# Kernel optimization log

Hardware: AMD Instinct MI355X
Metric: run time of the kernel (lower is better)

The kernel has to match this reference:

```python
import jax, jax.numpy as jnp
import numpy as np

# H2RConfig constants
KERNEL = 3
MAX_ROUTES = 1000
STRIDE = 4.0
MIN_SIZE = 32.0
MAX_SIZE = 512.0
SCORE_POWER = 2.0
UNC_WEIGHT = 0.35


def setup_inputs() -> dict:
    key = jax.random.key(0)
    k1, k2, k3 = jax.random.split(key, 3)
    shape = (32, 1, 512, 512)  # [B, 1, H, W] heatmaps at stride 4
    return {
        "route_logits": jax.random.normal(k1, shape, jnp.float32),
        "scale_logits": jax.random.normal(k2, shape, jnp.float32),
        "uncertainty_logits": jax.random.normal(k3, shape, jnp.float32),
        "image_h": 2048,
        "image_w": 2048,
    }


def reference(route_logits, scale_logits, uncertainty_logits, image_h, image_w):
    # score map: sigmoid^power, modulated by uncertainty (use_route_uncertainty=True)
    score = jnp.power(jax.nn.sigmoid(route_logits), SCORE_POWER)
    score = score * (1.0 - UNC_WEIGHT * jax.nn.sigmoid(uncertainty_logits))

    # local-max NMS: 3x3 max pool, stride 1, SAME padding (torch pads with -inf)
    pooled = jax.lax.reduce_window(
        score, -jnp.inf, jax.lax.max,
        window_dimensions=(1, 1, KERNEL, KERNEL),
        window_strides=(1, 1, 1, 1),
        padding="SAME",
    )
    peak_mask = score == pooled
    filtered = jnp.where(peak_mask, score, -1.0)

    B = score.shape[0]
    Wd = score.shape[3]
    flat = filtered.reshape(B, -1)                 # [B, H*W]
    values, indices = jax.lax.top_k(flat, MAX_ROUTES)  # [B, K]
    valid = values > 0.0                            # torch drops these; we mask/pad

    ys = indices // Wd
    xs = indices % Wd
    cx = (xs.astype(jnp.float32) + 0.5) * STRIDE
    cy = (ys.astype(jnp.float32) + 0.5) * STRIDE

    # gather scale / uncertainty at peak locations
    sc = jnp.take_along_axis(scale_logits.reshape(B, -1), indices, axis=1)
    un = jax.nn.sigmoid(jnp.take_along_axis(uncertainty_logits.reshape(B, -1), indices, axis=1))

    side = MIN_SIZE + jax.nn.sigmoid(sc) * (MAX_SIZE - MIN_SIZE)
    side = side * (1.0 + 0.25 * un)
    half = side * 0.5

    iw = float(image_w)
    ih = float(image_h)
    x1 = jnp.clip(cx - half, 0.0, iw - 1.0)
    y1 = jnp.clip(cy - half, 0.0, ih - 1.0)
    x2 = jnp.clip(cx + half, 1.0, iw)
    y2 = jnp.clip(cy + half, 1.0, ih)

    bcol = jnp.broadcast_to(jnp.arange(B, dtype=jnp.float32)[:, None], values.shape)
    rois = jnp.stack([bcol, x1, y1, x2, y2], axis=-1)  # [B, K, 5]

    # padded (fixed-shape) equivalent of torch's variable-length concat
    rois = jnp.where(valid[..., None], rois, 0.0)
    scores = jnp.where(valid, values, 0.0)
    return rois, scores, valid
```

## Files before the change

### kernel.cpp

```cpp
#include <hip/hip_runtime.h>
#include <hip/hip_bf16.h>
#include <math.h>


#define B_   32
#define H_   512
#define W_   512
#define HW_  (H_ * W_)
#define K_   1000
#define ROWS_ 16
#define THR_  512
#define NSTRIP_ 32
#define WSEGCAP_ 176
#define STRIPCAP_ (8 * WSEGCAP_)
#define NSLOT_ (NSTRIP_ * STRIPCAP_)
#define NPAIR_ (NSLOT_ / 2)
#define NBUK_ 4096
#define NW2_  (NBUK_ / 2)
#define GCAP_ 2048
#define HOTCAP_ 896
#define HOTPAIR_ (NSTRIP_ * HOTCAP_ / 2)
#define HOTBITS_ 0x3F000000u

#define PL_BYTES_  ((size_t)B_ * NSLOT_ * 8)
#define GH2_BYTES_ ((size_t)B_ * NSTRIP_ * NW2_ * 4)
#define HL_BYTES_  ((size_t)B_ * NSTRIP_ * HOTCAP_ * 8)

__device__ __forceinline__ float np_expf(float x) {
#pragma clang fp contract(off)
    const float log2e = 1.44269504088896341f;
    float z = x * log2e;
    float m = rintf(z);
    float r = fmaf(m, -0.693359375f, x);
    r = fmaf(m, 2.12194440e-4f, r);
    float r2 = r * r;
    float p = fmaf(1.9875691500e-4f, r, 1.3981999507e-3f);
    p = fmaf(p, r, 8.3334519073e-3f);
    p = fmaf(p, r, 4.1665795894e-2f);
    p = fmaf(p, r, 1.6666665459e-1f);
    p = fmaf(p, r, 5.0000001201e-1f);
    p = fmaf(p, r2, r);
    p = p + 1.0f;
    int mi = (int)m;
    float sc = __int_as_float((127 + mi) << 23);
    return p * sc;
}

__device__ __forceinline__ float sigmoid_np(float x) {
#pragma clang fp contract(off)
    float e = np_expf(-x);
    float d = 1.0f + e;
    return 1.0f / d;
}

__device__ __forceinline__ float score_ref(float r, float u) {
#pragma clang fp contract(off)
    float s  = sigmoid_np(r);
    float s2 = s * s;
    float su = sigmoid_np(u);
    float t  = 0.35f * su;
    float m  = 1.0f - t;
    return s2 * m;
}

__device__ __forceinline__ float sigmoid_fast(float x) {
    return 1.0f / (1.0f + __expf(-x));
}

__global__ __launch_bounds__(THR_, 4) void fused_peak_kernel(
    const float* __restrict__ route, const float* __restrict__ unc,
    unsigned long long* __restrict__ plist,
    unsigned int* __restrict__ ghist2,
    unsigned long long* __restrict__ hotlist)
{
    __shared__ float sm[ROWS_ + 2][W_];
    __shared__ int hcnt;

    const int tid   = threadIdx.x;
    const int lane  = tid & 63;
    const int wid   = tid >> 6;
    const int strip = blockIdx.x;
    const int b     = blockIdx.y;
    const int r0    = strip * ROWS_;
    if (tid == 0) hcnt = 0;

    const float4* rb4 = (const float4*)(route + (size_t)b * HW_);
    const float4* ub4 = (const float4*)(unc   + (size_t)b * HW_);
    unsigned long long* wseg =
        plist + (size_t)(b * NSTRIP_ + strip) * STRIPCAP_ + wid * WSEGCAP_;
    unsigned long long* hseg =
        hotlist + (size_t)(b * NSTRIP_ + strip) * HOTCAP_;

    float4 rv[5], uv[5];
    int lrow[5], c4[5]; bool ok[5];
    #pragma unroll
    for (int k = 0; k < 5; ++k) {
        int slot = tid + k * THR_;
        slot = slot < 2303 ? slot : 2303;
        int row = slot >> 7;
        int gy  = r0 - 1 + row;
        lrow[k] = row; c4[k] = slot & 127;
        ok[k]   = (gy >= 0 && gy < H_);
        int cy  = gy < 0 ? 0 : (gy >= H_ ? H_ - 1 : gy);
        rv[k] = rb4[cy * 128 + c4[k]];
        uv[k] = ub4[cy * 128 + c4[k]];
    }
    #pragma unroll
    for (int k = 0; k < 5; ++k) {
        float4 s;
        s.x = score_ref(rv[k].x, uv[k].x);
        s.y = score_ref(rv[k].y, uv[k].y);
        s.z = score_ref(rv[k].z, uv[k].z);
        s.w = score_ref(rv[k].w, uv[k].w);
        if (!ok[k]) { s.x = -INFINITY; s.y = -INFINITY;
                      s.z = -INFINITY; s.w = -INFINITY; }
        *(float4*)&sm[lrow[k]][c4[k] * 4] = s;
    }
    __syncthreads();

    const unsigned long long lt = (1ull << lane) - 1ull;
    int wn = 0;
    unsigned int hreg[8];
    #pragma unroll
    for (int j = 0; j < 4; ++j) {
        int g  = tid + j * THR_;
        int ly = 1 + (g >> 7);
        int x0 = (g & 127) * 4;
        int gy = r0 + (ly - 1);
        float4 q0 = *(const float4*)&sm[ly - 1][x0];
        float4 q1 = *(const float4*)&sm[ly    ][x0];
        float4 q2 = *(const float4*)&sm[ly + 1][x0];
        bool hasL = (x0 > 0), hasR = (x0 + 4 < W_);
        float l0 = hasL ? sm[ly - 1][x0 - 1] : -INFINITY;
        float l1 = hasL ? sm[ly    ][x0 - 1] : -INFINITY;
        float l2 = hasL ? sm[ly + 1][x0 - 1] : -INFINITY;
        float e0 = hasR ? sm[ly - 1][x0 + 4] : -INFINITY;
        float e1 = hasR ? sm[ly    ][x0 + 4] : -INFINITY;
        float e2 = hasR ? sm[ly + 1][x0 + 4] : -INFINITY;
        float f_m1 = fmaxf(l0, fmaxf(l1, l2));
        float f_0  = fmaxf(q0.x, fmaxf(q1.x, q2.x));
        float f_1  = fmaxf(q0.y, fmaxf(q1.y, q2.y));
        float f_2  = fmaxf(q0.z, fmaxf(q1.z, q2.z));
        float f_3  = fmaxf(q0.w, fmaxf(q1.w, q2.w));
        float f_4  = fmaxf(e0, fmaxf(e1, e2));
        float tb0  = fmaxf(q0.x, q2.x);
        float tb1  = fmaxf(q0.y, q2.y);
        float tb2  = fmaxf(q0.z, q2.z);
        float tb3  = fmaxf(q0.w, q2.w);
        float vv[4] = { q1.x, q1.y, q1.z, q1.w };
        float mm[4];
        mm[0] = fmaxf(fmaxf(f_m1, f_1), tb0);
        mm[1] = fmaxf(fmaxf(f_0,  f_2), tb1);
        mm[2] = fmaxf(fmaxf(f_1,  f_3), tb2);
        mm[3] = fmaxf(fmaxf(f_2,  f_4), tb3);
        unsigned int pk01 = 0u, pk23 = 0u;
        #pragma unroll
        for (int i = 0; i < 4; ++i) {
            bool take = (vv[i] >= mm[i]);
            unsigned long long mk = __ballot(take);
            int p = wn + __popcll(mk & lt);
            bool stored = take && (p < WSEGCAP_);
            unsigned int bits = __float_as_uint(vv[i]);
            unsigned long long key = 0ull;
            if (stored) {
                unsigned int idx = (unsigned int)(gy * W_ + x0 + i);
                key = ((unsigned long long)bits << 32)
                      | (0xFFFFFFFFu - idx);
                wseg[p] = key;
                unsigned int bkt = bits >> 18;
                if (i < 2) pk01 |= bkt << (16 * i);
                else       pk23 |= bkt << (16 * (i - 2));
            }
            bool hot = stored && (bits >= HOTBITS_);
            unsigned long long hmk = __ballot(hot);
            if (hmk) {
                int ldr = __ffsll(hmk) - 1;
                int hb = 0;
                if (lane == ldr) hb = atomicAdd(&hcnt, __popcll(hmk));
                hb = __shfl(hb, ldr, 64);
                if (hot) {
                    int hp = hb + __popcll(hmk & lt);
                    if (hp < HOTCAP_) hseg[hp] = key;
                }
            }
            wn += __popcll(mk);
        }
        hreg[2 * j]     = pk01;
        hreg[2 * j + 1] = pk23;
    }
    for (int i = (wn < WSEGCAP_ ? wn : WSEGCAP_) + lane; i < WSEGCAP_; i += 64)
        wseg[i] = 0ull;
    __syncthreads();

    {
        int hn = hcnt < HOTCAP_ ? hcnt : HOTCAP_;
        for (int i = hn + tid; i < HOTCAP_; i += THR_) hseg[i] = 0ull;
    }

    unsigned int* hist = (unsigned int*)&sm[0][0];
    for (int i = tid; i < NW2_; i += THR_) hist[i] = 0u;
    __syncthreads();

    #pragma unroll
    for (int j = 0; j < 8; ++j) {
        unsigned int h  = hreg[j];
        unsigned int b0 = h & 0xFFFFu;
        unsigned int b1 = h >> 16;
        if (b0) atomicAdd(&hist[b0 >> 1], 1u << ((b0 & 1) * 16));
        if (b1) atomicAdd(&hist[b1 >> 1], 1u << ((b1 & 1) * 16));
    }
    __syncthreads();

    unsigned int* gh2 = ghist2 + (size_t)(b * NSTRIP_ + strip) * NW2_;
    for (int i = tid; i < NW2_; i += THR_) gh2[i] = hist[i];
}

__global__ __launch_bounds__(1024) void select2_kernel(
    const float* __restrict__ scale, const float* __restrict__ unc,
    const unsigned long long* __restrict__ plist,
    const unsigned int* __restrict__ ghist2,
    const unsigned long long* __restrict__ hotlist,
    const int* __restrict__ ih_p, const int* __restrict__ iw_p,
    float* __restrict__ out)
{
    __shared__ unsigned int hist[NBUK_];
    __shared__ unsigned int cursor[NBUK_];
    __shared__ unsigned long long grp[GCAP_];
    __shared__ int sh_T, sh_nc, sh_fb;

    const int b = blockIdx.x, tid = threadIdx.x;
    const int lane = tid & 63, wid = tid >> 6;
    const unsigned int* gbase = ghist2 + (size_t)b * NSTRIP_ * NW2_;

    if (tid == 0) { sh_fb = 0; sh_T = 1; sh_nc = 0; }
    if (tid < 64) hist[NBUK_ - 64 + tid] = 0u;
    __syncthreads();
    {
        int s = tid >> 5;
        int w = (NW2_ - 32) + (tid & 31);
        unsigned int v = gbase[(size_t)s * NW2_ + w];
        int bkt = 2 * w;
        if (v & 0xFFFFu) atomicAdd(&hist[bkt],     v & 0xFFFFu);
        if (v >> 16)     atomicAdd(&hist[bkt + 1], v >> 16);
    }
    __syncthreads();

    if (wid == 0) {
        int cnt = (int)hist[NBUK_ - 64 + lane];
        int sum = cnt;
        #pragma unroll
        for (int off = 32; off > 0; off >>= 1)
            sum += __shfl_down(sum, off, 64);
        sum = __shfl(sum, 0, 64);
        if (sum < K_) {
            if (lane == 0) sh_fb = 1;
        } else {
            int suf = cnt;
            #pragma unroll
            for (int off = 1; off < 64; off <<= 1) {
                int o = __shfl_down(suf, off, 64);
                suf += (lane + off < 64) ? o : 0;
            }
            bool cond = suf >= K_;
            unsigned long long mask = __ballot(cond);
            int ls = 63 - __builtin_clzll(mask);
            int beta = NBUK_ - 64 + lane;
            if (lane >= ls) cursor[beta] = (unsigned int)(suf - cnt);
            int ncv = __shfl(suf, ls, 64);
            if (lane == 0) { sh_T = NBUK_ - 64 + ls; sh_nc = ncv; }
        }
    }
    __syncthreads();

    if (sh_fb) {
        for (int w = tid; w < NW2_; w += 1024) {
            unsigned int s0 = 0u, s1 = 0u;
            #pragma unroll
            for (int s = 0; s < NSTRIP_; ++s) {
                unsigned int v = gbase[s * NW2_ + w];
                s0 += v & 0xFFFFu;
                s1 += v >> 16;
            }
            hist[2 * w]     = s0;
            hist[2 * w + 1] = s1;
        }
        __syncthreads();
        if (wid == 0) {
            int Tv = 0;
            int total = 0;
            for (int c = NBUK_ / 64 - 1; c >= 0; --c) {
                int cnt = (int)hist[c * 64 + lane];
                int sum = cnt;
                #pragma unroll
                for (int off = 32; off > 0; off >>= 1)
                    sum += __shfl_down(sum, off, 64);
                sum = __shfl(sum, 0, 64);
                if (total + sum < K_) { total += sum; continue; }
                int suf = cnt;
                #pragma unroll
                for (int off = 1; off < 64; off <<= 1) {
                    int o = __shfl_down(suf, off, 64);
                    suf += (lane + off < 64) ? o : 0;
                }
                bool cond = (total + suf) >= K_;
                unsigned long long mask = __ballot(cond);
                int ls = 63 - __builtin_clzll(mask);
                Tv = c * 64 + ls;
                break;
            }
            if (Tv < 1) Tv = 1;
            int run = 0;
            for (int cb = NBUK_ - 64; cb >= (Tv & ~63); cb -= 64) {
                int beta = cb + lane;
                int cnt = (beta >= Tv) ? (int)hist[beta] : 0;
                int suf = cnt;
                #pragma unroll
                for (int off = 1; off < 64; off <<= 1) {
                    int o = __shfl_down(suf, off, 64);
                    suf += (lane + off < 64) ? o : 0;
                }
                int chunk_total = __shfl(suf, 0, 64);
                if (beta >= Tv) cursor[beta] = (unsigned int)(run + (suf - cnt));
                run += chunk_total;
            }
            if (lane == 0) { sh_T = Tv; sh_nc = run; }
        }
    }
    __syncthreads();
    const unsigned int T = (unsigned int)sh_T;
    const int fb = sh_fb;

    {
        const ulonglong2* src = fb
            ? (const ulonglong2*)(plist   + (size_t)b * NSLOT_)
            : (const ulonglong2*)(hotlist + (size_t)b * NSTRIP_ * HOTCAP_);
        const int npr = fb ? NPAIR_ : HOTPAIR_;
        for (int i = tid; i < npr; i += 1024) {
            ulonglong2 a = src[i];
            unsigned int b0 = (unsigned int)(a.x >> 50);
            unsigned int b1 = (unsigned int)(a.y >> 50);
            if (b0 >= T) {
                unsigned int pos = atomicAdd(&cursor[b0], 1u);
                if (pos < GCAP_) grp[pos] = a.x;
            }
            if (b1 >= T) {
                unsigned int pos = atomicAdd(&cursor[b1], 1u);
                if (pos < GCAP_) grp[pos] = a.y;
            }
        }
    }
    __syncthreads();

    const float fih = (float)(*ih_p);
    const float fiw = (float)(*iw_p);
    float* rois   = out;
    float* scores = out + (size_t)B_ * K_ * 5;
    float* validf = out + (size_t)B_ * K_ * 6;

    int nc = sh_nc;
    int ncEff = nc < GCAP_ ? nc : GCAP_;
    for (int p = tid; p < ncEff; p += 1024) {
        unsigned long long key = grp[p];
        unsigned int beta = (unsigned int)(key >> 50);
        int segEnd   = (int)cursor[beta];
        int segStart = segEnd - (int)hist[beta];
        int qEnd = segEnd < GCAP_ ? segEnd : GCAP_;
        int r = 0;
        for (int q = segStart; q < qEnd; ++q)
            r += (grp[q] > key) ? 1 : 0;
        int rank = segStart + r;
        if (rank < K_) {
            int o = b * K_ + rank;
            unsigned int bits = (unsigned int)(key >> 32);
            float v = __uint_as_float(bits);
            unsigned int idx = 0xFFFFFFFFu - (unsigned int)(key & 0xFFFFFFFFull);
            int y = (int)(idx >> 9), x = (int)(idx & 511u);
            float cx = ((float)x + 0.5f) * 4.0f;
            float cy = ((float)y + 0.5f) * 4.0f;
            float ss = sigmoid_fast(scale[(size_t)b * HW_ + idx]);
            float su = sigmoid_fast(unc  [(size_t)b * HW_ + idx]);
            float side = (32.0f + ss * 480.0f) * (1.0f + 0.25f * su);
            float half = 0.5f * side;
            float x1 = fminf(fmaxf(cx - half, 0.0f), fiw - 1.0f);
            float y1 = fminf(fmaxf(cy - half, 0.0f), fih - 1.0f);
            float x2 = fminf(fmaxf(cx + half, 1.0f), fiw);
            float y2 = fminf(fmaxf(cy + half, 1.0f), fih);
            rois[o * 5 + 0] = (float)b;
            rois[o * 5 + 1] = x1; rois[o * 5 + 2] = y1;
            rois[o * 5 + 3] = x2; rois[o * 5 + 4] = y2;
            scores[o] = v; validf[o] = 1.0f;
        }
    }
    for (int k = nc + tid; k < K_; k += 1024) {
        int o = b * K_ + k;
        rois[o * 5 + 0] = 0.0f; rois[o * 5 + 1] = 0.0f;
        rois[o * 5 + 2] = 0.0f; rois[o * 5 + 3] = 0.0f;
        rois[o * 5 + 4] = 0.0f;
        scores[o] = 0.0f; validf[o] = 0.0f;
    }
}

extern "C" void kernel_launch(void* const* d_in, const int* in_sizes, int n_in,
                              void* d_out, int out_size, void* d_ws, size_t ws_size,
                              hipStream_t stream) {
    const float* route = (const float*)d_in[0];
    const float* scale = (const float*)d_in[1];
    const float* unc   = (const float*)d_in[2];
    const int*   ih    = (const int*)d_in[3];
    const int*   iw    = (const int*)d_in[4];
    float* out = (float*)d_out;

    unsigned char* base = (unsigned char*)d_ws;
    unsigned long long* plist = (unsigned long long*)base;
    unsigned int* ghist2 = (unsigned int*)(base + PL_BYTES_);
    unsigned long long* hotlist =
        (unsigned long long*)(base + PL_BYTES_ + GH2_BYTES_);

    dim3 g(NSTRIP_, B_);
    fused_peak_kernel<<<g, THR_, 0, stream>>>(route, unc, plist, ghist2,
                                              hotlist);
    select2_kernel<<<B_, 1024, 0, stream>>>(scale, unc, plist, ghist2,
                                            hotlist, ih, iw, out);
}
```

Before: 164.6 us.

## Drop full peak list; recompute peaks in select kernel only on fallback

The peak kernel no longer writes every local-max key and a full 4096-bucket histogram per strip. It keeps only the hot list and a 64-bucket top histogram. The rare fallback path in the select kernel now recomputes scores and NMS for the whole image from the raw inputs, inside a single block per batch. This cuts global writes and shared-memory atomics on the common path, at the cost of a very slow fallback when fewer than K hot peaks exist.

```diff
diff --git a/kernel.cpp b/kernel.cpp
--- a/kernel.cpp
+++ b/kernel.cpp
@@ -11,20 +11,17 @@
 #define ROWS_ 16
 #define THR_  512
 #define NSTRIP_ 32
-#define WSEGCAP_ 176
-#define STRIPCAP_ (8 * WSEGCAP_)
-#define NSLOT_ (NSTRIP_ * STRIPCAP_)
-#define NPAIR_ (NSLOT_ / 2)
 #define NBUK_ 4096
-#define NW2_  (NBUK_ / 2)
 #define GCAP_ 2048
 #define HOTCAP_ 896
 #define HOTPAIR_ (NSTRIP_ * HOTCAP_ / 2)
 #define HOTBITS_ 0x3F000000u
-
-#define PL_BYTES_  ((size_t)B_ * NSLOT_ * 8)
-#define GH2_BYTES_ ((size_t)B_ * NSTRIP_ * NW2_ * 4)
+#define WBASE_ (NBUK_ - 64)
+#define FBCAP_ 45056
+
 #define HL_BYTES_  ((size_t)B_ * NSTRIP_ * HOTCAP_ * 8)
+#define GW_BYTES_  ((size_t)B_ * NSTRIP_ * 64 * 4)
+#define FB_BYTES_  ((size_t)B_ * FBCAP_ * 8)
 
 __device__ __forceinline__ float np_expf(float x) {
 #pragma clang fp contract(off)
@@ -69,25 +66,23 @@
 
 __global__ __launch_bounds__(THR_, 4) void fused_peak_kernel(
     const float* __restrict__ route, const float* __restrict__ unc,
-    unsigned long long* __restrict__ plist,
-    unsigned int* __restrict__ ghist2,
-    unsigned long long* __restrict__ hotlist)
+    unsigned long long* __restrict__ hotlist,
+    unsigned int* __restrict__ ghw)
 {
     __shared__ float sm[ROWS_ + 2][W_];
+    __shared__ unsigned int whist[64];
     __shared__ int hcnt;
 
     const int tid   = threadIdx.x;
     const int lane  = tid & 63;
-    const int wid   = tid >> 6;
     const int strip = blockIdx.x;
     const int b     = blockIdx.y;
     const int r0    = strip * ROWS_;
+    if (tid < 64) whist[tid] = 0u;
     if (tid == 0) hcnt = 0;
 
     const float4* rb4 = (const float4*)(route + (size_t)b * HW_);
     const float4* ub4 = (const float4*)(unc   + (size_t)b * HW_);
-    unsigned long long* wseg =
-        plist + (size_t)(b * NSTRIP_ + strip) * STRIPCAP_ + wid * WSEGCAP_;
     unsigned long long* hseg =
         hotlist + (size_t)(b * NSTRIP_ + strip) * HOTCAP_;
 
@@ -119,8 +114,6 @@
     __syncthreads();
 
     const unsigned long long lt = (1ull << lane) - 1ull;
-    int wn = 0;
-    unsigned int hreg[8];
     #pragma unroll
     for (int j = 0; j < 4; ++j) {
         int g  = tid + j * THR_;
@@ -153,25 +146,11 @@
         mm[1] = fmaxf(fmaxf(f_0,  f_2), tb1);
         mm[2] = fmaxf(fmaxf(f_1,  f_3), tb2);
         mm[3] = fmaxf(fmaxf(f_2,  f_4), tb3);
-        unsigned int pk01 = 0u, pk23 = 0u;
         #pragma unroll
         for (int i = 0; i < 4; ++i) {
             bool take = (vv[i] >= mm[i]);
-            unsigned long long mk = __ballot(take);
-            int p = wn + __popcll(mk & lt);
-            bool stored = take && (p < WSEGCAP_);
             unsigned int bits = __float_as_uint(vv[i]);
-            unsigned long long key = 0ull;
-            if (stored) {
-                unsigned int idx = (unsigned int)(gy * W_ + x0 + i);
-                key = ((unsigned long long)bits << 32)
-                      | (0xFFFFFFFFu - idx);
-                wseg[p] = key;
-                unsigned int bkt = bits >> 18;
-                if (i < 2) pk01 |= bkt << (16 * i);
-                else       pk23 |= bkt << (16 * (i - 2));
-            }
-            bool hot = stored && (bits >= HOTBITS_);
+            bool hot = take && (bits >= HOTBITS_);
             unsigned long long hmk = __ballot(hot);
             if (hmk) {
                 int ldr = __ffsll(hmk) - 1;
@@ -180,73 +159,60 @@
                 hb = __shfl(hb, ldr, 64);
                 if (hot) {
                     int hp = hb + __popcll(hmk & lt);
-                    if (hp < HOTCAP_) hseg[hp] = key;
+                    if (hp < HOTCAP_) {
+                        unsigned int idx = (unsigned int)(gy * W_ + x0 + i);
+                        hseg[hp] = ((unsigned long long)bits << 32)
+                                   | (0xFFFFFFFFu - idx);
+                        atomicAdd(&whist[(bits >> 18) - WBASE_], 1u);
+                    }
                 }
             }
-            wn += __popcll(mk);
-        }
-        hreg[2 * j]     = pk01;
-        hreg[2 * j + 1] = pk23;
-    }
-    for (int i = (wn < WSEGCAP_ ? wn : WSEGCAP_) + lane; i < WSEGCAP_; i += 64)
-        wseg[i] = 0ull;
+        }
+    }
     __syncthreads();
 
     {
         int hn = hcnt < HOTCAP_ ? hcnt : HOTCAP_;
         for (int i = hn + tid; i < HOTCAP_; i += THR_) hseg[i] = 0ull;
     }
-
-    unsigned int* hist = (unsigned int*)&sm[0][0];
-    for (int i = tid; i < NW2_; i += THR_) hist[i] = 0u;
-    __syncthreads();
-
-    #pragma unroll
-    for (int j = 0; j < 8; ++j) {
-        unsigned int h  = hreg[j];
-        unsigned int b0 = h & 0xFFFFu;
-        unsigned int b1 = h >> 16;
-        if (b0) atomicAdd(&hist[b0 >> 1], 1u << ((b0 & 1) * 16));
-        if (b1) atomicAdd(&hist[b1 >> 1], 1u << ((b1 & 1) * 16));
-    }
-    __syncthreads();
-
-    unsigned int* gh2 = ghist2 + (size_t)(b * NSTRIP_ + strip) * NW2_;
-    for (int i = tid; i < NW2_; i += THR_) gh2[i] = hist[i];
+    if (tid < 64)
+        ghw[(size_t)(b * NSTRIP_ + strip) * 64 + tid] = whist[tid];
 }
 
 __global__ __launch_bounds__(1024) void select2_kernel(
+    const float* __restrict__ route, const float* __restrict__ unc_r,
     const float* __restrict__ scale, const float* __restrict__ unc,
-    const unsigned long long* __restrict__ plist,
-    const unsigned int* __restrict__ ghist2,
     const unsigned long long* __restrict__ hotlist,
+    const unsigned int* __restrict__ ghw,
+    unsigned long long* __restrict__ fbbuf,
     const int* __restrict__ ih_p, const int* __restrict__ iw_p,
     float* __restrict__ out)
 {
+    __shared__ __align__(16) unsigned char u_[(ROWS_ + 2) * W_ * 4];
     __shared__ unsigned int hist[NBUK_];
-    __shared__ unsigned int cursor[NBUK_];
-    __shared__ unsigned long long grp[GCAP_];
-    __shared__ int sh_T, sh_nc, sh_fb;
+    __shared__ int sh_T, sh_nc, sh_fb, sh_fn;
+
+    float (*sm)[W_] = (float (*)[W_])u_;
+    unsigned int* cursor = (unsigned int*)u_;
+    unsigned long long* grp = (unsigned long long*)(u_ + 16384);
 
     const int b = blockIdx.x, tid = threadIdx.x;
     const int lane = tid & 63, wid = tid >> 6;
-    const unsigned int* gbase = ghist2 + (size_t)b * NSTRIP_ * NW2_;
-
-    if (tid == 0) { sh_fb = 0; sh_T = 1; sh_nc = 0; }
-    if (tid < 64) hist[NBUK_ - 64 + tid] = 0u;
+
+    if (tid == 0) { sh_fb = 0; sh_T = 1; sh_nc = 0; sh_fn = 0; }
+    if (tid < 64) hist[WBASE_ + tid] = 0u;
     __syncthreads();
     {
-        int s = tid >> 5;
-        int w = (NW2_ - 32) + (tid & 31);
-        unsigned int v = gbase[(size_t)s * NW2_ + w];
-        int bkt = 2 * w;
-        if (v & 0xFFFFu) atomicAdd(&hist[bkt],     v & 0xFFFFu);
-        if (v >> 16)     atomicAdd(&hist[bkt + 1], v >> 16);
+        const unsigned int* gw = ghw + (size_t)b * NSTRIP_ * 64;
+        for (int i = tid; i < NSTRIP_ * 64; i += 1024) {
+            unsigned int v = gw[i];
+            if (v) atomicAdd(&hist[WBASE_ + (i & 63)], v);
+        }
     }
     __syncthreads();
 
     if (wid == 0) {
-        int cnt = (int)hist[NBUK_ - 64 + lane];
+        int cnt = (int)hist[WBASE_ + lane];
         int sum = cnt;
         #pragma unroll
         for (int off = 32; off > 0; off >>= 1)
@@ -264,27 +230,94 @@
             bool cond = suf >= K_;
             unsigned long long mask = __ballot(cond);
             int ls = 63 - __builtin_clzll(mask);
-            int beta = NBUK_ - 64 + lane;
-            if (lane >= ls) cursor[beta] = (unsigned int)(suf - cnt);
+            if (lane >= ls) cursor[WBASE_ + lane] = (unsigned int)(suf - cnt);
             int ncv = __shfl(suf, ls, 64);
-            if (lane == 0) { sh_T = NBUK_ - 64 + ls; sh_nc = ncv; }
-        }
-    }
-    __syncthreads();
-
-    if (sh_fb) {
-        for (int w = tid; w < NW2_; w += 1024) {
-            unsigned int s0 = 0u, s1 = 0u;
-            #pragma unroll
-            for (int s = 0; s < NSTRIP_; ++s) {
-                unsigned int v = gbase[s * NW2_ + w];
-                s0 += v & 0xFFFFu;
-                s1 += v >> 16;
-            }
-            hist[2 * w]     = s0;
-            hist[2 * w + 1] = s1;
-        }
+            if (lane == 0) { sh_T = WBASE_ + ls; sh_nc = ncv; }
+        }
+    }
+    __syncthreads();
+    const int fb = sh_fb;
+
+    if (fb) {
+        for (int i = tid; i < NBUK_; i += 1024) hist[i] = 0u;
         __syncthreads();
+
+        const float4* rb4 = (const float4*)(route + (size_t)b * HW_);
+        const float4* ub4 = (const float4*)(unc_r + (size_t)b * HW_);
+        unsigned long long* fbb = fbbuf + (size_t)b * FBCAP_;
+
+        for (int strip = 0; strip < NSTRIP_; ++strip) {
+            const int r0 = strip * ROWS_;
+            __syncthreads();
+            for (int slot = tid; slot < 2304; slot += 1024) {
+                int row = slot >> 7;
+                int gy  = r0 - 1 + row;
+                int c4  = slot & 127;
+                bool okr = (gy >= 0 && gy < H_);
+                int cy  = gy < 0 ? 0 : (gy >= H_ - 1 ? H_ - 1 : gy);
+                float4 r4 = rb4[cy * 128 + c4];
+                float4 u4 = ub4[cy * 128 + c4];
+                float4 s;
+                s.x = score_ref(r4.x, u4.x);
+                s.y = score_ref(r4.y, u4.y);
+                s.z = score_ref(r4.z, u4.z);
+                s.w = score_ref(r4.w, u4.w);
+                if (!okr) { s.x = -INFINITY; s.y = -INFINITY;
+                            s.z = -INFINITY; s.w = -INFINITY; }
+                *(float4*)&sm[row][c4 * 4] = s;
+            }
+            __syncthreads();
+            for (int g = tid; g < 4 * 512; g += 1024) {
+                int ly = 1 + (g >> 7);
+                (void)ly;
+            }
+            for (int g = tid; g < 2048; g += 1024) {
+                int ly = 1 + (g >> 7);
+                int x0 = (g & 127) * 4;
+                int gy = r0 + (ly - 1);
+                float4 q0 = *(const float4*)&sm[ly - 1][x0];
+                float4 q1 = *(const float4*)&sm[ly    ][x0];
+                float4 q2 = *(const float4*)&sm[ly + 1][x0];
+                bool hasL = (x0 > 0), hasR = (x0 + 4 < W_);
+                float l0 = hasL ? sm[ly - 1][x0 - 1] : -INFINITY;
+                float l1 = hasL ? sm[ly    ][x0 - 1] : -INFINITY;
+                float l2 = hasL ? sm[ly + 1][x0 - 1] : -INFINITY;
+                float e0 = hasR ? sm[ly - 1][x0 + 4] : -INFINITY;
+                float e1 = hasR ? sm[ly    ][x0 + 4] : -INFINITY;
+                float e2 = hasR ? sm[ly + 1][x0 + 4] : -INFINITY;
+                float f_m1 = fmaxf(l0, fmaxf(l1, l2));
+                float f_0  = fmaxf(q0.x, fmaxf(q1.x, q2.x));
+                float f_1  = fmaxf(q0.y, fmaxf(q1.y, q2.y));
+                float f_2  = fmaxf(q0.z, fmaxf(q1.z, q2.z));
+                float f_3  = fmaxf(q0.w, fmaxf(q1.w, q2.w));
+                float f_4  = fmaxf(e0, fmaxf(e1, e2));
+                float tb0  = fmaxf(q0.x, q2.x);
+                float tb1  = fmaxf(q0.y, q2.y);
+                float tb2  = fmaxf(q0.z, q2.z);
+                float tb3  = fmaxf(q0.w, q2.w);
+                float vv[4] = { q1.x, q1.y, q1.z, q1.w };
+                float mm[4];
+                mm[0] = fmaxf(fmaxf(f_m1, f_1), tb0);
+                mm[1] = fmaxf(fmaxf(f_0,  f_2), tb1);
+                mm[2] = fmaxf(fmaxf(f_1,  f_3), tb2);
+                mm[3] = fmaxf(fmaxf(f_2,  f_4), tb3);
+                #pragma unroll
+                for (int i = 0; i < 4; ++i) {
+                    if (vv[i] >= mm[i]) {
+                        unsigned int bits = __float_as_uint(vv[i]);
+                        unsigned int idx  = (unsigned int)(gy * W_ + x0 + i);
+                        int p = atomicAdd(&sh_fn, 1);
+                        if (p < FBCAP_) {
+                            fbb[p] = ((unsigned long long)bits << 32)
+                                     | (0xFFFFFFFFu - idx);
+                            atomicAdd(&hist[bits >> 18], 1u);
+                        }
+                    }
+                }
+            }
+        }
+        __syncthreads();
+
         if (wid == 0) {
             int Tv = 0;
             int total = 0;
@@ -328,14 +361,11 @@
     }
     __syncthreads();
     const unsigned int T = (unsigned int)sh_T;
-    const int fb = sh_fb;
-
-    {
-        const ulonglong2* src = fb
-            ? (const ulonglong2*)(plist   + (size_t)b * NSLOT_)
-            : (const ulonglong2*)(hotlist + (size_t)b * NSTRIP_ * HOTCAP_);
-        const int npr = fb ? NPAIR_ : HOTPAIR_;
-        for (int i = tid; i < npr; i += 1024) {
+
+    if (!fb) {
+        const ulonglong2* src =
+            (const ulonglong2*)(hotlist + (size_t)b * NSTRIP_ * HOTCAP_);
+        for (int i = tid; i < HOTPAIR_; i += 1024) {
             ulonglong2 a = src[i];
             unsigned int b0 = (unsigned int)(a.x >> 50);
             unsigned int b1 = (unsigned int)(a.y >> 50);
@@ -346,6 +376,17 @@
             if (b1 >= T) {
                 unsigned int pos = atomicAdd(&cursor[b1], 1u);
                 if (pos < GCAP_) grp[pos] = a.y;
+            }
+        }
+    } else {
+        const unsigned long long* fbb = fbbuf + (size_t)b * FBCAP_;
+        int n = sh_fn; if (n > FBCAP_) n = FBCAP_;
+        for (int i = tid; i < n; i += 1024) {
+            unsigned long long k = fbb[i];
+            unsigned int b0 = (unsigned int)(k >> 50);
+            if (b0 >= T) {
+                unsigned int pos = atomicAdd(&cursor[b0], 1u);
+                if (pos < GCAP_) grp[pos] = k;
             }
         }
     }
@@ -411,14 +452,14 @@
     float* out = (float*)d_out;
 
     unsigned char* base = (unsigned char*)d_ws;
-    unsigned long long* plist = (unsigned long long*)base;
-    unsigned int* ghist2 = (unsigned int*)(base + PL_BYTES_);
-    unsigned long long* hotlist =
-        (unsigned long long*)(base + PL_BYTES_ + GH2_BYTES_);
+    unsigned long long* hotlist = (unsigned long long*)base;
+    unsigned int* ghw = (unsigned int*)(base + HL_BYTES_);
+    unsigned long long* fbbuf =
+        (unsigned long long*)(base + HL_BYTES_ + GW_BYTES_);
 
     dim3 g(NSTRIP_, B_);
-    fused_peak_kernel<<<g, THR_, 0, stream>>>(route, unc, plist, ghist2,
-                                              hotlist);
-    select2_kernel<<<B_, 1024, 0, stream>>>(scale, unc, plist, ghist2,
-                                            hotlist, ih, iw, out);
-}
+    fused_peak_kernel<<<g, THR_, 0, stream>>>(route, unc, hotlist, ghw);
+    select2_kernel<<<B_, 1024, 0, stream>>>(route, unc, scale, unc,
+                                            hotlist, ghw, fbbuf,
+                                            ih, iw, out);
+}
```

Result: faster. 158.6 us (-3.7%).
